# Kernel optimization log

Measured on AMD Instinct MI355X. Metric: run time of the kernel, lower is better.

Reference implementation:

```python
import jax, jax.numpy as jnp
import numpy as np

B, T, C, H = 2, 2048, 1024, 16
HD = C // H  # head dim = 64


def setup_inputs() -> dict:
    key = jax.random.key(0)
    ks = jax.random.split(key, 9)
    s = 1.0 / np.sqrt(C)
    return {
        "x": jax.random.normal(ks[0], (B, T, C), dtype=jnp.float32),
        "Wq": jax.random.normal(ks[1], (C, C), dtype=jnp.float32) * s,
        "bq": jax.random.normal(ks[2], (C,), dtype=jnp.float32) * 0.02,
        "Wk": jax.random.normal(ks[3], (C, C), dtype=jnp.float32) * s,
        "bk": jax.random.normal(ks[4], (C,), dtype=jnp.float32) * 0.02,
        "Wv": jax.random.normal(ks[5], (C, C), dtype=jnp.float32) * s,
        "bv": jax.random.normal(ks[6], (C,), dtype=jnp.float32) * 0.02,
        "Wo": jax.random.normal(ks[7], (C, C), dtype=jnp.float32) * s,
        "bo": jax.random.normal(ks[8], (C,), dtype=jnp.float32) * 0.02,
    }


def reference(x, Wq, bq, Wk, bk, Wv, bv, Wo, bo):
    # Projections (torch Linear: x @ W.T + b; here W stored pre-transposed as [C_in, C_out])
    q = x @ Wq + bq  # (B,T,C)
    k = x @ Wk + bk
    v = x @ Wv + bv
    # Split heads: (B,T,C) -> (B,H,T,HD)
    q = q.reshape(B, T, H, HD).transpose(0, 2, 1, 3)
    k = k.reshape(B, T, H, HD).transpose(0, 2, 1, 3)
    v = v.reshape(B, T, H, HD).transpose(0, 2, 1, 3)
    # NOTE: original module never applies a causal mask despite its name.
    score = jnp.einsum("bhqd,bhkd->bhqk", q, k) / jnp.sqrt(jnp.float32(HD))
    score = jax.nn.softmax(score, axis=-1)
    y = jnp.einsum("bhqk,bhkd->bhqd", score, v)
    y = y.transpose(0, 2, 1, 3).reshape(B, T, C)
    # dropout is identity in eval mode
    return y @ Wo + bo
```

## Files before the change

### kernel.cpp

```cpp
#include <hip/hip_runtime.h>
#include <math.h>

#define B_ 2
#define T_ 2048
#define C_ 1024
#define H_ 16
#define HD_ 64
#define M_ (B_*T_)

typedef _Float16 half2v __attribute__((ext_vector_type(2)));
typedef _Float16 half4v __attribute__((ext_vector_type(4)));
typedef _Float16 half8v __attribute__((ext_vector_type(8)));
typedef float f32x4 __attribute__((ext_vector_type(4)));

#define GLD_LDS(gp, lp) \
  __builtin_amdgcn_global_load_lds( \
      (const __attribute__((address_space(1))) void*)(gp), \
      (__attribute__((address_space(3))) void*)(lp), 16, 0, 0)

__global__ __launch_bounds__(256) void prep_kernel(
    const float* __restrict__ x,
    const float* __restrict__ Wq, const float* __restrict__ Wk,
    const float* __restrict__ Wv, const float* __restrict__ Wo,
    const float* __restrict__ bq, const float* __restrict__ bk,
    const float* __restrict__ bv,
    _Float16* __restrict__ xh, _Float16* __restrict__ Wt3,
    _Float16* __restrict__ Wot, float* __restrict__ b3)
{
  __shared__ float tile[32][33];
  const int blk = blockIdx.x, thr = threadIdx.x;
  if (blk < 2048) {
    int base = blk * 512;
    float4 v0 = ((const float4*)x)[base + thr];
    float4 v1 = ((const float4*)x)[base + 256 + thr];
    half4v h0, h1;
    h0[0] = (_Float16)v0.x; h0[1] = (_Float16)v0.y;
    h0[2] = (_Float16)v0.z; h0[3] = (_Float16)v0.w;
    h1[0] = (_Float16)v1.x; h1[1] = (_Float16)v1.y;
    h1[2] = (_Float16)v1.z; h1[3] = (_Float16)v1.w;
    ((half4v*)xh)[base + thr] = h0;
    ((half4v*)xh)[base + 256 + thr] = h1;
  } else if (blk < 6144) {
    int zz = (blk - 2048) >> 10;
    int bxy = (blk - 2048) & 1023;
    const float* W; _Float16* Wt;
    switch (zz) {
      case 0:  W = Wq; Wt = Wt3; break;
      case 1:  W = Wk; Wt = Wt3 + (size_t)1024 * 1024; break;
      case 2:  W = Wv; Wt = Wt3 + (size_t)2048 * 1024; break;
      default: W = Wo; Wt = Wot; break;
    }
    const int n0 = (bxy & 31) * 32, k0 = (bxy >> 5) * 32;
    const int tx = thr & 31, ty = thr >> 5;
#pragma unroll
    for (int r = 0; r < 4; r++) {
      int k = ty + r * 8;
      tile[k][tx] = W[(size_t)(k0 + k) * C_ + n0 + tx];
    }
    __syncthreads();
#pragma unroll
    for (int r = 0; r < 4; r++) {
      int n = ty + r * 8;
      Wt[(size_t)(n0 + n) * C_ + k0 + tx] = (_Float16)tile[tx][n];
    }
  } else {
    int i = (blk - 6144) * 256 + thr;
    const float* s = (i < 1024) ? bq : ((i < 2048) ? bk : bv);
    b3[i] = s[i & 1023];
  }
}

template <int BM, int BN, int EPI, int GX, int GY>
__global__ __launch_bounds__(256) void gemm_f16_kernel(
    const _Float16* __restrict__ A, const _Float16* __restrict__ Bw,
    const float* __restrict__ bias,
    _Float16* __restrict__ o0, _Float16* __restrict__ o1,
    _Float16* __restrict__ o2, float* __restrict__ of)
{
  constexpr int FM = BM / 32, FN = BN / 32;
  constexpr int NWG = GX * GY, CPX = NWG / 8;
  __shared__ __align__(16) _Float16 As[2 * BM * 32];
  __shared__ __align__(16) _Float16 Bs[2 * BN * 32];
  const int t = threadIdx.x;
  const int w = t >> 6, lane = t & 63, l15 = lane & 15, quad = lane >> 4;
  const int wm = (w & 1) * (BM / 2), wn = (w >> 1) * (BN / 2);
  const int lin = blockIdx.x + GX * blockIdx.y;
  const int swz = (lin & 7) * CPX + (lin >> 3);
  const int bxs = swz % GX, bys = swz / GX;
  const int bm = bys * BM, bn = bxs * BN;
  const int lrow = lane >> 2, lcol = (lane & 3) * 8;

  f32x4 acc[FM][FN];
#pragma unroll
  for (int i = 0; i < FM; i++)
#pragma unroll
    for (int j = 0; j < FN; j++) acc[i][j] = (f32x4){0.f, 0.f, 0.f, 0.f};

  for (int k0 = 0; k0 < 1024; k0 += 64) {
#pragma unroll
    for (int hf = 0; hf < 2; hf++) {
#pragma unroll
      for (int i = 0; i < BM / 64; i++) {
        int ca = w + 4 * i;
        int row = ca * 16 + lrow;
        GLD_LDS(A + (size_t)(bm + row) * 1024 + k0 + hf * 32 + lcol,
                As + hf * BM * 32 + ca * 512);
      }
#pragma unroll
      for (int i = 0; i < BN / 64; i++) {
        int cb = w + 4 * i;
        int row = cb * 16 + lrow;
        GLD_LDS(Bw + (size_t)(bn + row) * 1024 + k0 + hf * 32 + lcol,
                Bs + hf * BN * 32 + cb * 512);
      }
    }
    __syncthreads();

#pragma unroll
    for (int hf = 0; hf < 2; hf++) {
      half8v af[FM], bf[FN];
#pragma unroll
      for (int mt = 0; mt < FM; mt++)
        af[mt] = *(const half8v*)(As + hf * BM * 32 +
                                  (wm + mt * 16 + l15) * 32 + quad * 8);
#pragma unroll
      for (int nt = 0; nt < FN; nt++)
        bf[nt] = *(const half8v*)(Bs + hf * BN * 32 +
                                  (wn + nt * 16 + l15) * 32 + quad * 8);
#pragma unroll
      for (int mt = 0; mt < FM; mt++)
#pragma unroll
        for (int nt = 0; nt < FN; nt++)
          acc[mt][nt] = __builtin_amdgcn_mfma_f32_16x16x32_f16(
              af[mt], bf[nt], acc[mt][nt], 0, 0, 0);
    }
    __syncthreads();
  }

#pragma unroll
  for (int mt = 0; mt < FM; mt++)
#pragma unroll
    for (int nt = 0; nt < FN; nt++) {
      int n = bn + wn + nt * 16 + l15;
      float bv = bias[n];
      if (EPI == 0 && bn >= 2048) {
        int dg = n - 2048;
        int hh = dg >> 6, hd = dg & 63;
        int m0 = bm + wm + mt * 16 + quad * 4;
        int bb = m0 >> 11, tt = m0 & 2047;
        half2v p01 = __builtin_bit_cast(half2v,
            __builtin_amdgcn_cvt_pkrtz(acc[mt][nt][0] + bv, acc[mt][nt][1] + bv));
        half2v p23 = __builtin_bit_cast(half2v,
            __builtin_amdgcn_cvt_pkrtz(acc[mt][nt][2] + bv, acc[mt][nt][3] + bv));
        half4v pk = __builtin_shufflevector(p01, p23, 0, 1, 2, 3);
        *(half4v*)(o2 + (((size_t)(bb * H_ + hh) * 64 + hd) * 2048 + tt)) = pk;
      } else {
#pragma unroll
        for (int r = 0; r < 4; r++) {
          int m = bm + wm + mt * 16 + quad * 4 + r;
          float v = acc[mt][nt][r] + bv;
          if (EPI == 0) {
            if (bn < 1024) {
              o0[(size_t)m * 1024 + n] = (_Float16)(v * 0.180336884f);
            } else {
              o1[(size_t)m * 1024 + (n - 1024)] = (_Float16)v;
            }
          } else {
            of[(size_t)m * 1024 + n] = v;
          }
        }
      }
    }
}

__global__ __launch_bounds__(512) void attn_f16_kernel(
    const _Float16* __restrict__ Qh, const _Float16* __restrict__ Kh,
    const _Float16* __restrict__ Vt, _Float16* __restrict__ Yh)
{
  __shared__ __align__(16) _Float16 Ks[128 * 68];
  __shared__ __align__(16) _Float16 Vs[64 * 132];
  const int t = threadIdx.x;
  const int w = t >> 6, lane = t & 63, l15 = lane & 15, quad = lane >> 4;
  const int lin = blockIdx.x + 16 * blockIdx.y + 256 * blockIdx.z;
  const int swz = (lin & 7) * 64 + (lin >> 3);
  const int qt = swz & 15, h = (swz >> 4) & 15, b = swz >> 8;
  const int qg = qt * 128 + w * 16 + l15;
  const size_t qoff = ((size_t)(b * T_ + qg)) * C_ + h * HD_;

  half8v qf[2];
  qf[0] = *(const half8v*)(Qh + qoff + quad * 8);
  qf[1] = *(const half8v*)(Qh + qoff + 32 + quad * 8);

  f32x4 o[4];
#pragma unroll
  for (int i = 0; i < 4; i++) o[i] = (f32x4){0.f, 0.f, 0.f, 0.f};
  float m_run = -INFINITY, l_run = 0.f;

  const size_t kbase = ((size_t)b * T_) * C_ + h * HD_;
  const size_t vbase = ((size_t)(b * H_ + h)) * HD_ * 2048;

  for (int kt0 = 0; kt0 < T_; kt0 += 128) {
#pragma unroll
    for (int i = 0; i < 2; i++) {
      int slot = t + i * 512;
      int row = slot >> 3, cp = slot & 7;
      *(uint4*)((char*)Ks + row * 136 + cp * 16) =
          *(const uint4*)(Kh + kbase + (size_t)(kt0 + row) * C_ + cp * 8);
    }
#pragma unroll
    for (int i = 0; i < 2; i++) {
      int slot = t + i * 512;
      int row = slot >> 4, cp = slot & 15;
      *(uint4*)((char*)Vs + row * 264 + cp * 16) =
          *(const uint4*)(Vt + vbase + (size_t)row * 2048 + kt0 + cp * 8);
    }
    __syncthreads();

    f32x4 s[8];
    __builtin_amdgcn_s_setprio(1);
#pragma unroll
    for (int kt = 0; kt < 8; kt++) {
      s[kt] = (f32x4){0.f, 0.f, 0.f, 0.f};
      int key = kt * 16 + l15;
#pragma unroll
      for (int ks = 0; ks < 2; ks++) {
        half8v kf = *(const half8v*)((char*)Ks + key * 136 + (ks * 4 + quad) * 16);
        s[kt] = __builtin_amdgcn_mfma_f32_16x16x32_f16(kf, qf[ks], s[kt], 0, 0, 0);
      }
    }
    __builtin_amdgcn_s_setprio(0);

    float tmax = -INFINITY;
#pragma unroll
    for (int kt = 0; kt < 8; kt++)
#pragma unroll
      for (int r = 0; r < 4; r++) tmax = fmaxf(tmax, s[kt][r]);
    tmax = fmaxf(tmax, __shfl_xor(tmax, 16));
    tmax = fmaxf(tmax, __shfl_xor(tmax, 32));
    float mnew = fmaxf(m_run, tmax);
    float alpha = __builtin_amdgcn_exp2f(m_run - mnew);

    float psum = 0.f;
    half4v pf[8];
#pragma unroll
    for (int kt = 0; kt < 8; kt++) {
      float p0 = __builtin_amdgcn_exp2f(s[kt][0] - mnew);
      float p1 = __builtin_amdgcn_exp2f(s[kt][1] - mnew);
      float p2 = __builtin_amdgcn_exp2f(s[kt][2] - mnew);
      float p3 = __builtin_amdgcn_exp2f(s[kt][3] - mnew);
      psum += (p0 + p1) + (p2 + p3);
      half2v pk01 = __builtin_bit_cast(half2v, __builtin_amdgcn_cvt_pkrtz(p0, p1));
      half2v pk23 = __builtin_bit_cast(half2v, __builtin_amdgcn_cvt_pkrtz(p2, p3));
      pf[kt] = __builtin_shufflevector(pk01, pk23, 0, 1, 2, 3);
    }
    psum += __shfl_xor(psum, 16);
    psum += __shfl_xor(psum, 32);
    l_run = l_run * alpha + psum;
    m_run = mnew;
#pragma unroll
    for (int dt = 0; dt < 4; dt++) o[dt] *= alpha;

    __builtin_amdgcn_s_setprio(1);
#pragma unroll
    for (int dt = 0; dt < 4; dt++) {
      int d = dt * 16 + l15;
#pragma unroll
      for (int p = 0; p < 4; p++) {
        half4v v0 = *(const half4v*)((char*)Vs + d * 264 + p * 64 + quad * 8);
        half4v v1 = *(const half4v*)((char*)Vs + d * 264 + p * 64 + 32 + quad * 8);
        half8v vf = __builtin_shufflevector(v0, v1, 0, 1, 2, 3, 4, 5, 6, 7);
        half8v pf8 = __builtin_shufflevector(pf[2 * p], pf[2 * p + 1],
                                             0, 1, 2, 3, 4, 5, 6, 7);
        o[dt] = __builtin_amdgcn_mfma_f32_16x16x32_f16(vf, pf8, o[dt], 0, 0, 0);
      }
    }
    __builtin_amdgcn_s_setprio(0);
    __syncthreads();
  }

  float inv = 1.0f / l_run;
#pragma unroll
  for (int dt = 0; dt < 4; dt++) {
    half4v yv;
#pragma unroll
    for (int r = 0; r < 4; r++) yv[r] = (_Float16)(o[dt][r] * inv);
    *(half4v*)(Yh + qoff + dt * 16 + quad * 4) = yv;
  }
}

extern "C" void kernel_launch(void* const* d_in, const int* in_sizes, int n_in,
                              void* d_out, int out_size, void* d_ws, size_t ws_size,
                              hipStream_t stream) {
  const float* x  = (const float*)d_in[0];
  const float* Wq = (const float*)d_in[1];
  const float* bq = (const float*)d_in[2];
  const float* Wk = (const float*)d_in[3];
  const float* bk = (const float*)d_in[4];
  const float* Wv = (const float*)d_in[5];
  const float* bv = (const float*)d_in[6];
  const float* Wo = (const float*)d_in[7];
  const float* bo = (const float*)d_in[8];
  float* out = (float*)d_out;

  char* ws = (char*)d_ws;
  _Float16* xh   = (_Float16*)(ws);
  _Float16* Qh   = (_Float16*)(ws + (((size_t)8)  << 20));
  _Float16* Kh   = (_Float16*)(ws + (((size_t)16) << 20));
  _Float16* Vt   = (_Float16*)(ws + (((size_t)24) << 20));
  _Float16* Yh   = (_Float16*)(ws + (((size_t)32) << 20));
  _Float16* Wt3  = (_Float16*)(ws + (((size_t)40) << 20));
  _Float16* Wot  = (_Float16*)(ws + (((size_t)46) << 20));
  float*    b3   = (float*)   (ws + (((size_t)48) << 20));

  prep_kernel<<<6156, 256, 0, stream>>>(x, Wq, Wk, Wv, Wo, bq, bk, bv,
                                        xh, Wt3, Wot, b3);

  gemm_f16_kernel<128, 128, 0, 24, 32><<<dim3(24, 32), 256, 0, stream>>>(
      xh, Wt3, b3, Qh, Kh, Vt, nullptr);

  attn_f16_kernel<<<dim3(T_ / 128, H_, B_), 512, 0, stream>>>(Qh, Kh, Vt, Yh);

  gemm_f16_kernel<64, 128, 1, 8, 64><<<dim3(8, 64), 256, 0, stream>>>(
      Yh, Wot, bo, nullptr, nullptr, nullptr, out);
}
```

Measured before the change: 196.1 us.

## Split attention over two key halves and merge partials in a combine kernel

Attention gets a split-K (flash-decoding style) mode. Each block processes half of the key sequence and writes unnormalized fp32 partial outputs plus running max and sum to workspace, and a new combine kernel rescales and merges the two halves into fp16 Y. This doubles the attention grid from 512 to 1024 blocks to fill the GPU's compute units better. In exchange it adds an extra launch and about 32MB of fp32 partial writes and reads. The path runs only when the workspace is large enough.

```diff
diff --git a/kernel.cpp b/kernel.cpp
--- a/kernel.cpp
+++ b/kernel.cpp
@@ -173,17 +173,23 @@
     }
 }
 
+template <int SPLIT>
 __global__ __launch_bounds__(512) void attn_f16_kernel(
     const _Float16* __restrict__ Qh, const _Float16* __restrict__ Kh,
-    const _Float16* __restrict__ Vt, _Float16* __restrict__ Yh)
+    const _Float16* __restrict__ Vt, _Float16* __restrict__ Yh,
+    float* __restrict__ Op, float2* __restrict__ mlp)
 {
   __shared__ __align__(16) _Float16 Ks[128 * 68];
   __shared__ __align__(16) _Float16 Vs[64 * 132];
   const int t = threadIdx.x;
   const int w = t >> 6, lane = t & 63, l15 = lane & 15, quad = lane >> 4;
   const int lin = blockIdx.x + 16 * blockIdx.y + 256 * blockIdx.z;
-  const int swz = (lin & 7) * 64 + (lin >> 3);
-  const int qt = swz & 15, h = (swz >> 4) & 15, b = swz >> 8;
+  const int swz = SPLIT ? ((lin & 7) * 128 + (lin >> 3))
+                        : ((lin & 7) * 64 + (lin >> 3));
+  const int qt = swz & 15, h = (swz >> 4) & 15;
+  const int zz = swz >> 8;
+  const int b = SPLIT ? (zz >> 1) : zz;
+  const int half = SPLIT ? (zz & 1) : 0;
   const int qg = qt * 128 + w * 16 + l15;
   const size_t qoff = ((size_t)(b * T_ + qg)) * C_ + h * HD_;
 
@@ -199,7 +205,10 @@
   const size_t kbase = ((size_t)b * T_) * C_ + h * HD_;
   const size_t vbase = ((size_t)(b * H_ + h)) * HD_ * 2048;
 
-  for (int kt0 = 0; kt0 < T_; kt0 += 128) {
+  const int kt_lo = SPLIT ? half * 1024 : 0;
+  const int kt_hi = SPLIT ? kt_lo + 1024 : T_;
+
+  for (int kt0 = kt_lo; kt0 < kt_hi; kt0 += 128) {
 #pragma unroll
     for (int i = 0; i < 2; i++) {
       int slot = t + i * 512;
@@ -278,14 +287,57 @@
     __syncthreads();
   }
 
-  float inv = 1.0f / l_run;
-#pragma unroll
-  for (int dt = 0; dt < 4; dt++) {
-    half4v yv;
-#pragma unroll
-    for (int r = 0; r < 4; r++) yv[r] = (_Float16)(o[dt][r] * inv);
-    *(half4v*)(Yh + qoff + dt * 16 + quad * 4) = yv;
-  }
+  if (SPLIT) {
+    const int row = b * T_ + qg;
+    float* op = Op + (size_t)half * 4194304 + (size_t)row * 1024 + h * HD_;
+#pragma unroll
+    for (int dt = 0; dt < 4; dt++) {
+      float4 pv;
+      pv.x = o[dt][0]; pv.y = o[dt][1]; pv.z = o[dt][2]; pv.w = o[dt][3];
+      *(float4*)(op + dt * 16 + quad * 4) = pv;
+    }
+    if (quad == 0) {
+      float2 ml; ml.x = m_run; ml.y = l_run;
+      mlp[(size_t)half * 65536 + (size_t)row * 16 + h] = ml;
+    }
+  } else {
+    float inv = 1.0f / l_run;
+#pragma unroll
+    for (int dt = 0; dt < 4; dt++) {
+      half4v yv;
+#pragma unroll
+      for (int r = 0; r < 4; r++) yv[r] = (_Float16)(o[dt][r] * inv);
+      *(half4v*)(Yh + qoff + dt * 16 + quad * 4) = yv;
+    }
+  }
+}
+
+__global__ __launch_bounds__(256) void attn_combine(
+    const float* __restrict__ Op, const float2* __restrict__ mlp,
+    _Float16* __restrict__ Yh)
+{
+  const int idx = blockIdx.x * 256 + threadIdx.x;
+  const int row = idx >> 7;
+  const int c0  = (idx & 127) * 8;
+  const int h   = c0 >> 6;
+  float2 ml0 = mlp[(size_t)row * 16 + h];
+  float2 ml1 = mlp[(size_t)65536 + (size_t)row * 16 + h];
+  float M  = fmaxf(ml0.x, ml1.x);
+  float a0 = __builtin_amdgcn_exp2f(ml0.x - M);
+  float a1 = __builtin_amdgcn_exp2f(ml1.x - M);
+  float inv = 1.0f / (ml0.y * a0 + ml1.y * a1);
+  const float4* p0 = (const float4*)(Op + (size_t)row * 1024 + c0);
+  const float4* p1 = (const float4*)(Op + (size_t)4194304 + (size_t)row * 1024 + c0);
+  half8v y;
+#pragma unroll
+  for (int i = 0; i < 2; i++) {
+    float4 u = p0[i], v = p1[i];
+    y[i * 4 + 0] = (_Float16)((u.x * a0 + v.x * a1) * inv);
+    y[i * 4 + 1] = (_Float16)((u.y * a0 + v.y * a1) * inv);
+    y[i * 4 + 2] = (_Float16)((u.z * a0 + v.z * a1) * inv);
+    y[i * 4 + 3] = (_Float16)((u.w * a0 + v.w * a1) * inv);
+  }
+  *(half8v*)(Yh + (size_t)row * 1024 + c0) = y;
 }
 
 extern "C" void kernel_launch(void* const* d_in, const int* in_sizes, int n_in,
@@ -311,6 +363,9 @@
   _Float16* Wt3  = (_Float16*)(ws + (((size_t)40) << 20));
   _Float16* Wot  = (_Float16*)(ws + (((size_t)46) << 20));
   float*    b3   = (float*)   (ws + (((size_t)48) << 20));
+  float*    Op   = (float*)   (ws + (((size_t)56) << 20));
+  float2*   mlp  = (float2*)  (ws + (((size_t)88) << 20));
+  const bool split_ok = ws_size >= (((size_t)90) << 20);
 
   prep_kernel<<<6156, 256, 0, stream>>>(x, Wq, Wk, Wv, Wo, bq, bk, bv,
                                         xh, Wt3, Wot, b3);
@@ -318,7 +373,14 @@
   gemm_f16_kernel<128, 128, 0, 24, 32><<<dim3(24, 32), 256, 0, stream>>>(
       xh, Wt3, b3, Qh, Kh, Vt, nullptr);
 
-  attn_f16_kernel<<<dim3(T_ / 128, H_, B_), 512, 0, stream>>>(Qh, Kh, Vt, Yh);
+  if (split_ok) {
+    attn_f16_kernel<1><<<dim3(T_ / 128, H_, 2 * B_), 512, 0, stream>>>(
+        Qh, Kh, Vt, Yh, Op, mlp);
+    attn_combine<<<2048, 256, 0, stream>>>(Op, mlp, Yh);
+  } else {
+    attn_f16_kernel<0><<<dim3(T_ / 128, H_, B_), 512, 0, stream>>>(
+        Qh, Kh, Vt, Yh, nullptr, nullptr);
+  }
 
   gemm_f16_kernel<64, 128, 1, 8, 64><<<dim3(8, 64), 256, 0, stream>>>(
       Yh, Wot, bo, nullptr, nullptr, nullptr, out);
```

New measurement: 208.2 us. 6.2% more time.
